# Kernel tuning notes

Measured on AMD Instinct MI355X. Metric: run time of the kernel, lower is better.

The kernel has to match this reference:

```python
import jax, jax.numpy as jnp
import numpy as np

EMBED_DIM = 1024
NUM_HEADS = 16
HEAD_SIZE = EMBED_DIM // NUM_HEADS  # 64
MAX_EMBED_DIM = 2048
MAX_HEAD_SIZE = 128
B, T = 4, 2048


def setup_inputs() -> dict:
    key = jax.random.key(0)
    kx, kq, kk, kv = jax.random.split(key, 4)
    x = jax.random.normal(kx, (B, T, MAX_EMBED_DIM), dtype=jnp.float32)
    # base-head weights sized for the max config; slices are taken in reference()
    Wq = jax.random.normal(kq, (NUM_HEADS, MAX_HEAD_SIZE, MAX_EMBED_DIM), dtype=jnp.float32) * 0.02
    Wk = jax.random.normal(kk, (NUM_HEADS, MAX_HEAD_SIZE, MAX_EMBED_DIM), dtype=jnp.float32) * 0.02
    Wv = jax.random.normal(kv, (NUM_HEADS, MAX_HEAD_SIZE, MAX_EMBED_DIM), dtype=jnp.float32) * 0.02
    return {"x": x, "Wq": Wq, "Wk": Wk, "Wv": Wv}


def reference(x, Wq, Wk, Wv):
    Bx, Tx, _ = x.shape
    xs = x[:, :, :EMBED_DIM]                       # [B, T, E]
    # slice sampled sub-weights: [H, d, E]
    wq = Wq[:, :HEAD_SIZE, :EMBED_DIM]
    wk = Wk[:, :HEAD_SIZE, :EMBED_DIM]
    wv = Wv[:, :HEAD_SIZE, :EMBED_DIM]
    q = jnp.einsum('bte,hde->bhtd', xs, wq)        # [B, H, T, d]
    k = jnp.einsum('bte,hde->bhtd', xs, wk)
    v = jnp.einsum('bte,hde->bhtd', xs, wv)
    scale = jnp.asarray(HEAD_SIZE, x.dtype) ** -0.5
    wei = jnp.einsum('bhtd,bhsd->bhts', q, k) * scale   # [B, H, T, T]
    causal = jnp.tril(jnp.ones((Tx, Tx), dtype=bool))
    wei = jnp.where(causal, wei, jnp.asarray(-jnp.inf, wei.dtype))
    wei = jax.nn.softmax(wei, axis=-1)
    # dropout is identity in eval mode
    out = jnp.einsum('bhts,bhsd->bhtd', wei, v)    # [B, H, T, d]
    out = out.transpose(0, 2, 1, 3).reshape(Bx, Tx, NUM_HEADS * HEAD_SIZE)
    pad = MAX_EMBED_DIM - NUM_HEADS * HEAD_SIZE
    return jnp.pad(out, ((0, 0), (0, 0), (0, pad)))
```

## Files before the change

### kernel.cpp

```cpp
#include <hip/hip_runtime.h>

typedef __attribute__((ext_vector_type(8))) short bf16x8;
typedef __attribute__((ext_vector_type(4))) float f32x4;
typedef __attribute__((ext_vector_type(16))) float f32x16;
typedef __attribute__((ext_vector_type(8))) unsigned short u16x8;
typedef __attribute__((ext_vector_type(4))) unsigned int u32x4;

#define TT 2048

__device__ __forceinline__ unsigned short f2bf(float f) {
  unsigned int u = __builtin_bit_cast(unsigned int, f);
  u += 0x7FFFu + ((u >> 16) & 1u);
  return (unsigned short)(u >> 16);
}

__device__ __forceinline__ void gld16(const void* g, void* l) {
  __builtin_amdgcn_global_load_lds((const __attribute__((address_space(1))) void*)g,
                                   (__attribute__((address_space(3))) void*)l, 16, 0, 0);
}

__device__ __forceinline__ unsigned int cvtpk(float lo, float hi) {
  unsigned int r;
  asm("v_cvt_pk_bf16_f32 %0, %1, %2" : "=v"(r) : "v"(lo), "v"(hi));
  return r;
}

__device__ __forceinline__ void pl32swap(unsigned int& a, unsigned int& b) {
  asm volatile("v_permlane32_swap_b32 %0, %1" : "+v"(a), "+v"(b));
}

__global__ __launch_bounds__(256) void conv_all(const float* __restrict__ x,
                                                const float* __restrict__ Wq,
                                                const float* __restrict__ Wk,
                                                const float* __restrict__ Wv,
                                                unsigned short* __restrict__ xb,
                                                unsigned short* __restrict__ wb) {
  const int bid = blockIdx.x;
  const float* src;
  unsigned short* dst;
  size_t idx;
  if (bid < 4096) {
    idx = ((size_t)bid * 256 + threadIdx.x) * 8;
    const int m = (int)(idx >> 10);
    const int e = (int)(idx & 1023);
    src = x + (size_t)m * 2048 + e;
    dst = xb + idx;
  } else {
    idx = ((size_t)(bid - 4096) * 256 + threadIdx.x) * 8;
    const int n = (int)(idx >> 10);
    const int e = (int)(idx & 1023);
    const int mat = n >> 10, hh = (n >> 6) & 15, d = n & 63;
    const float* W = (mat == 0) ? Wq : ((mat == 1) ? Wk : Wv);
    src = W + ((size_t)hh * 128 + d) * 2048 + e;
    dst = wb + idx;
  }
  const float4* s = (const float4*)src;
  float4 a = s[0], b = s[1];
  u16x8 v;
  v[0]=f2bf(a.x); v[1]=f2bf(a.y); v[2]=f2bf(a.z); v[3]=f2bf(a.w);
  v[4]=f2bf(b.x); v[5]=f2bf(b.y); v[6]=f2bf(b.z); v[7]=f2bf(b.w);
  *(u16x8*)dst = v;
}

__global__ __launch_bounds__(256, 3) void qkv_gemm5(const unsigned short* __restrict__ xb,
                                                    const unsigned short* __restrict__ wb,
                                                    unsigned short* __restrict__ Q,
                                                    unsigned short* __restrict__ Kt,
                                                    unsigned short* __restrict__ Vt) {
  __shared__ unsigned short As[3][64 * 64];
  __shared__ unsigned short Bs[3][64 * 64];
  const int tid = threadIdx.x;
  const int w = tid >> 6, lane = tid & 63, g = lane >> 4, c = lane & 15;
  const int wm = w >> 1, wn = w & 1;
  const int m0 = blockIdx.x * 128;
  const int n0 = blockIdx.y * 128;

  size_t aoff[2], boff[2];
  int lofs[2];
#pragma unroll
  for (int it = 0; it < 2; ++it) {
    const int o = (it * 256 + tid) * 16;
    const int row = o >> 7, stored = o & 127;
    const int logical = stored ^ ((row & 7) << 4);
    const int seg = logical >> 6, kb = logical & 63;
    const int m = row + (seg << 6);
    aoff[it] = ((size_t)(m0 + m) << 10) + (kb >> 1);
    boff[it] = ((size_t)(n0 + m) << 10) + (kb >> 1);
    lofs[it] = o;
  }
  int ardo[4], brdo[4];
#pragma unroll
  for (int mi = 0; mi < 4; ++mi) {
    const int m = wm * 64 + mi * 16 + c;
    const int row = m & 63, seg = m >> 6;
    ardo[mi] = row * 128 + (((seg << 6) + (g << 4)) ^ ((row & 7) << 4));
    const int n = wn * 64 + mi * 16 + c;
    const int nrow = n & 63, nseg = n >> 6;
    brdo[mi] = nrow * 128 + (((nseg << 6) + (g << 4)) ^ ((nrow & 7) << 4));
  }

  f32x4 acc[4][4];
#pragma unroll
  for (int mi = 0; mi < 4; ++mi)
#pragma unroll
    for (int ni = 0; ni < 4; ++ni) acc[mi][ni] = (f32x4){0.f, 0.f, 0.f, 0.f};

  auto STAGE = [&](int k0, int buf) {
#pragma unroll
    for (int it = 0; it < 2; ++it) {
      gld16(xb + aoff[it] + k0, (char*)&As[buf][0] + lofs[it]);
      gld16(wb + boff[it] + k0, (char*)&Bs[buf][0] + lofs[it]);
    }
  };

  STAGE(0, 0);
  STAGE(32, 1);
  asm volatile("s_waitcnt vmcnt(4)" ::: "memory");
  __builtin_amdgcn_s_barrier();

  int b0 = 0, b1 = 1, b2 = 2;
  for (int t = 0; t < 32; ++t) {
    const bool more = (t + 2 < 32);
    if (more) STAGE((t + 2) * 32, b2);
    bf16x8 af[4], bfv[4];
#pragma unroll
    for (int mi = 0; mi < 4; ++mi) {
      af[mi]  = *(const bf16x8*)((const char*)&As[b0][0] + ardo[mi]);
      bfv[mi] = *(const bf16x8*)((const char*)&Bs[b0][0] + brdo[mi]);
    }
    __builtin_amdgcn_s_setprio(1);
#pragma unroll
    for (int mi = 0; mi < 4; ++mi)
#pragma unroll
      for (int ni = 0; ni < 4; ++ni)
        acc[mi][ni] = __builtin_amdgcn_mfma_f32_16x16x32_bf16(af[mi], bfv[ni], acc[mi][ni], 0, 0, 0);
    __builtin_amdgcn_s_setprio(0);
    if (more) asm volatile("s_waitcnt vmcnt(4)" ::: "memory");
    else      asm volatile("s_waitcnt vmcnt(0)" ::: "memory");
    __builtin_amdgcn_s_barrier();
    const int tmp = b0; b0 = b1; b1 = b2; b2 = tmp;
  }

#pragma unroll
  for (int mi = 0; mi < 4; ++mi) {
    const int row_l = wm * 64 + mi * 16 + g * 4;
#pragma unroll
    for (int i = 0; i < 4; ++i) {
      const int m = m0 + row_l + i;
      const int b = m >> 11, tt = m & 2047;
#pragma unroll
      for (int ni = 0; ni < 4; ++ni) {
        const int n = n0 + wn * 64 + ni * 16 + c;
        const int mat = n >> 10, hh = (n >> 6) & 15, d = n & 63;
        const unsigned short v = f2bf(acc[mi][ni][i]);
        const size_t bh = (size_t)(b * 16 + hh);
        if (mat == 0)      Q [(bh * TT + tt) * 64 + d] = v;
        else if (mat == 1) Kt[(bh * TT + tt) * 64 + d] = v;
        else               Vt[(bh * 64 + d) * TT + tt] = v;
      }
    }
  }
}

__global__ __launch_bounds__(256) void attn4(const unsigned short* __restrict__ Q,
                                             const unsigned short* __restrict__ K,
                                             const unsigned short* __restrict__ Vt,
                                             float* __restrict__ out) {
  __shared__ unsigned short Ks[2][4096];
  __shared__ unsigned short Vs[2][4096];
  const int blk = blockIdx.x;
  const int bh = blk & 63;
  const int qi = 15 - (blk >> 6);
  const int b = bh >> 4, h = bh & 15;
  const int tid = threadIdx.x;
  const int w = tid >> 6, lane = tid & 63;
  const int ql = lane & 31;
  const int hi = lane >> 5, hi8 = hi * 8;
  const int q0 = qi * 128;
  const int qw = q0 + w * 32;
  const int q = qw + ql;
  const unsigned short* Qp = Q  + (size_t)bh * TT * 64;
  const unsigned short* Kp = K  + (size_t)bh * TT * 64;
  const unsigned short* Vp = Vt + (size_t)bh * 64 * TT;

  bf16x8 qf0, qf1, qf2, qf3;
  {
    const unsigned short* qa = Qp + (size_t)q * 64 + hi8;
    qf0 = *(const bf16x8*)(qa);
    qf1 = *(const bf16x8*)(qa + 16);
    qf2 = *(const bf16x8*)(qa + 32);
    qf3 = *(const bf16x8*)(qa + 48);
  }

  f32x16 o0, o1;
#pragma unroll
  for (int r = 0; r < 16; ++r) { o0[r] = 0.f; o1[r] = 0.f; }
  float m = -3.0e38f, l = 0.f;
  const float c2 = 0.125f * 1.44269504f;

  const int nt = qi * 2 + 2;

  auto STAGE = [&](int t, int buf) {
#pragma unroll
    for (int it = 0; it < 2; ++it) {
      const int o = (it * 256 + tid) * 16;
      const int r = o >> 7, c = o & 127;
      const int cs = c ^ ((r & 7) << 4);
      gld16(Kp + (size_t)t * 4096 + r * 64 + (cs >> 1), (char*)&Ks[buf][0] + o);
      gld16(Vp + (size_t)r * 2048 + t * 64 + (cs >> 1), (char*)&Vs[buf][0] + o);
    }
  };

  STAGE(0, 0);
  asm volatile("s_waitcnt vmcnt(0)" ::: "memory");
  __syncthreads();

  int cur = 0;
  for (int t = 0; t < nt; ++t) {
    if (t + 1 < nt) STAGE(t + 1, cur ^ 1);

#pragma unroll
    for (int s = 0; s < 2; ++s) {
      const int ks32 = t * 64 + s * 32;
      if (ks32 <= qw) {
        const int krow = s * 32 + ql;
        const char* kb = (const char*)&Ks[cur][krow * 64];
        const int ksz = (krow & 7) << 4;
        bf16x8 kf0 = *(const bf16x8*)(kb + ((0  + hi * 16) ^ ksz));
        bf16x8 kf1 = *(const bf16x8*)(kb + ((32 + hi * 16) ^ ksz));
        bf16x8 kf2 = *(const bf16x8*)(kb + ((64 + hi * 16) ^ ksz));
        bf16x8 kf3 = *(const bf16x8*)(kb + ((96 + hi * 16) ^ ksz));
        const int vsz = (ql & 7) << 4;
        const char* vb0 = (const char*)&Vs[cur][ql * 64];
        const char* vb1 = (const char*)&Vs[cur][(ql + 32) * 64];
        bf16x8 vf0 = *(const bf16x8*)(vb0 + ((s * 64 + 0  + hi * 16) ^ vsz));
        bf16x8 vf1 = *(const bf16x8*)(vb0 + ((s * 64 + 32 + hi * 16) ^ vsz));
        bf16x8 vf2 = *(const bf16x8*)(vb1 + ((s * 64 + 0  + hi * 16) ^ vsz));
        bf16x8 vf3 = *(const bf16x8*)(vb1 + ((s * 64 + 32 + hi * 16) ^ vsz));

        f32x16 st;
#pragma unroll
        for (int r = 0; r < 16; ++r) st[r] = 0.f;
        __builtin_amdgcn_s_setprio(1);
        st = __builtin_amdgcn_mfma_f32_32x32x16_bf16(kf0, qf0, st, 0, 0, 0);
        st = __builtin_amdgcn_mfma_f32_32x32x16_bf16(kf1, qf1, st, 0, 0, 0);
        st = __builtin_amdgcn_mfma_f32_32x32x16_bf16(kf2, qf2, st, 0, 0, 0);
        st = __builtin_amdgcn_mfma_f32_32x32x16_bf16(kf3, qf3, st, 0, 0, 0);
        __builtin_amdgcn_s_setprio(0);

        if (ks32 == qw) {
#pragma unroll
          for (int r = 0; r < 16; ++r) {
            const int krw = (r & 3) + 8 * (r >> 2) + 4 * hi;
            if (krw > ql) st[r] = -3.0e38f;
          }
        }

        float t0 = fmaxf(st[0], st[1]),  t1 = fmaxf(st[2], st[3]);
        float t2 = fmaxf(st[4], st[5]),  t3 = fmaxf(st[6], st[7]);
        float t4 = fmaxf(st[8], st[9]),  t5 = fmaxf(st[10], st[11]);
        float t6 = fmaxf(st[12], st[13]), t7 = fmaxf(st[14], st[15]);
        t0 = fmaxf(t0, t1); t2 = fmaxf(t2, t3); t4 = fmaxf(t4, t5); t6 = fmaxf(t6, t7);
        float pm = fmaxf(fmaxf(t0, t2), fmaxf(t4, t6));
        pm = fmaxf(pm, __shfl_xor(pm, 32));
        if (!__all(pm - m <= 44.36f)) {
          const float mnew = fmaxf(m, pm);
          const float alpha = __builtin_amdgcn_exp2f((m - mnew) * c2);
          m = mnew;
          l *= alpha;
#pragma unroll
          for (int r = 0; r < 16; ++r) { o0[r] *= alpha; o1[r] *= alpha; }
        }
        float p[16];
        float rs = 0.f;
#pragma unroll
        for (int r = 0; r < 16; ++r) {
          p[r] = __builtin_amdgcn_exp2f((st[r] - m) * c2);
          rs += p[r];
        }
        rs += __shfl_xor(rs, 32);
        l += rs;

        unsigned int a0 = cvtpk(p[0], p[1]),  a1 = cvtpk(p[2], p[3]);
        unsigned int b0 = cvtpk(p[4], p[5]),  b1 = cvtpk(p[6], p[7]);
        pl32swap(a0, b0); pl32swap(a1, b1);
        unsigned int cc0 = cvtpk(p[8], p[9]),  cc1 = cvtpk(p[10], p[11]);
        unsigned int dd0 = cvtpk(p[12], p[13]), dd1 = cvtpk(p[14], p[15]);
        pl32swap(cc0, dd0); pl32swap(cc1, dd1);
        u32x4 pw0 = {a0, a1, b0, b1};
        u32x4 pw1 = {cc0, cc1, dd0, dd1};
        bf16x8 pf0 = __builtin_bit_cast(bf16x8, pw0);
        bf16x8 pf1 = __builtin_bit_cast(bf16x8, pw1);

        __builtin_amdgcn_s_setprio(1);
        o0 = __builtin_amdgcn_mfma_f32_32x32x16_bf16(vf0, pf0, o0, 0, 0, 0);
        o0 = __builtin_amdgcn_mfma_f32_32x32x16_bf16(vf1, pf1, o0, 0, 0, 0);
        o1 = __builtin_amdgcn_mfma_f32_32x32x16_bf16(vf2, pf0, o1, 0, 0, 0);
        o1 = __builtin_amdgcn_mfma_f32_32x32x16_bf16(vf3, pf1, o1, 0, 0, 0);
        __builtin_amdgcn_s_setprio(0);
      }
    }

    asm volatile("s_waitcnt vmcnt(0)" ::: "memory");
    __syncthreads();
    cur ^= 1;
  }

  const float inv = 1.f / l;
  float* ob = out + ((size_t)b * TT + q) * 2048 + h * 64;
#pragma unroll
  for (int r = 0; r < 16; ++r) {
    const int row = (r & 3) + 8 * (r >> 2) + 4 * hi;
    ob[row]      = o0[r] * inv;
    ob[32 + row] = o1[r] * inv;
  }

  const float4 z = make_float4(0.f, 0.f, 0.f, 0.f);
#pragma unroll
  for (int it = 0; it < 8; ++it) {
    const int idx = it * 256 + tid;
    const int r = idx >> 4, c4 = idx & 15;
    *((float4*)(out + ((size_t)b * TT + q0 + r) * 2048 + 1024 + h * 64) + c4) = z;
  }
}

extern "C" void kernel_launch(void* const* d_in, const int* in_sizes, int n_in,
                              void* d_out, int out_size, void* d_ws, size_t ws_size,
                              hipStream_t stream) {
  const float* x  = (const float*)d_in[0];
  const float* Wq = (const float*)d_in[1];
  const float* Wk = (const float*)d_in[2];
  const float* Wv = (const float*)d_in[3];

  unsigned short* wsp = (unsigned short*)d_ws;
  unsigned short* Q   = wsp;
  unsigned short* Kt  = wsp + (size_t)8388608;
  unsigned short* Vt  = wsp + (size_t)16777216;

  unsigned short* xb = (unsigned short*)d_out;
  unsigned short* wb = (unsigned short*)((char*)d_out + 33554432);
  float* out = (float*)d_out;

  conv_all<<<5632, 256, 0, stream>>>(x, Wq, Wk, Wv, xb, wb);
  qkv_gemm5<<<dim3(64, 24), 256, 0, stream>>>(xb, wb, Q, Kt, Vt);
  attn4<<<1024, 256, 0, stream>>>(Q, Kt, Vt, out);
}
```

Before: 168.0 us.

## Rewrite QKV GEMM with 256x256 tiles, 8 waves, and interleaved load/MFMA phases

Replaces the 128x128 triple-buffered QKV projection GEMM with a 256x256 tile kernel using 512 threads (8 waves, each computing 128x64) and double-buffered K=64 stages split into four interleaved load/compute phases. A block-index swizzle groups tiles for better L2 reuse of the A and B panels. The larger tile raises arithmetic intensity and cuts redundant global reads. In exchange it uses more registers and LDS per block, adds more barriers per iteration, and launches only 384 blocks, so there is less occupancy to hide latency.

Measured after the change: 175.3 us. 1.04x slower.

```diff
diff --git a/kernel.cpp b/kernel.cpp
--- a/kernel.cpp
+++ b/kernel.cpp
@@ -62,88 +62,135 @@
   *(u16x8*)dst = v;
 }
 
-__global__ __launch_bounds__(256, 3) void qkv_gemm5(const unsigned short* __restrict__ xb,
-                                                    const unsigned short* __restrict__ wb,
-                                                    unsigned short* __restrict__ Q,
-                                                    unsigned short* __restrict__ Kt,
-                                                    unsigned short* __restrict__ Vt) {
-  __shared__ unsigned short As[3][64 * 64];
-  __shared__ unsigned short Bs[3][64 * 64];
+__global__ __launch_bounds__(512) void qkv_gemm8(const unsigned short* __restrict__ xb,
+                                                 const unsigned short* __restrict__ wb,
+                                                 unsigned short* __restrict__ Q,
+                                                 unsigned short* __restrict__ Kt,
+                                                 unsigned short* __restrict__ Vt) {
+  __shared__ unsigned short As[2][2][8192];
+  __shared__ unsigned short Bs[2][2][8192];
   const int tid = threadIdx.x;
   const int w = tid >> 6, lane = tid & 63, g = lane >> 4, c = lane & 15;
-  const int wm = w >> 1, wn = w & 1;
-  const int m0 = blockIdx.x * 128;
-  const int n0 = blockIdx.y * 128;
+  const int wm = w >> 2, wn = w & 3;
+  const int bid = blockIdx.x;
+  const int swz = (bid & 7) * 48 + (bid >> 3);
+  const int m0 = (swz / 12) * 256;
+  const int n0 = (swz % 12) * 256;
 
   size_t aoff[2], boff[2];
   int lofs[2];
 #pragma unroll
   for (int it = 0; it < 2; ++it) {
-    const int o = (it * 256 + tid) * 16;
-    const int row = o >> 7, stored = o & 127;
-    const int logical = stored ^ ((row & 7) << 4);
+    const int o = (it * 512 + tid) * 16;
+    const int lr = o >> 7;
+    const int logical = (o & 127) ^ ((lr & 7) << 4);
     const int seg = logical >> 6, kb = logical & 63;
-    const int m = row + (seg << 6);
-    aoff[it] = ((size_t)(m0 + m) << 10) + (kb >> 1);
-    boff[it] = ((size_t)(n0 + m) << 10) + (kb >> 1);
+    const int r = lr + (seg << 7);
+    aoff[it] = (size_t)(m0 + r) * 1024 + (kb >> 1);
+    boff[it] = (size_t)(n0 + r) * 1024 + (kb >> 1);
     lofs[it] = o;
   }
-  int ardo[4], brdo[4];
-#pragma unroll
-  for (int mi = 0; mi < 4; ++mi) {
-    const int m = wm * 64 + mi * 16 + c;
-    const int row = m & 63, seg = m >> 6;
-    ardo[mi] = row * 128 + (((seg << 6) + (g << 4)) ^ ((row & 7) << 4));
-    const int n = wn * 64 + mi * 16 + c;
-    const int nrow = n & 63, nseg = n >> 6;
-    brdo[mi] = nrow * 128 + (((nseg << 6) + (g << 4)) ^ ((nrow & 7) << 4));
-  }
-
-  f32x4 acc[4][4];
-#pragma unroll
-  for (int mi = 0; mi < 4; ++mi)
+  int abyte[8], bbyte[4];
+#pragma unroll
+  for (int mi = 0; mi < 8; ++mi) {
+    const int r = wm * 128 + mi * 16 + c;
+    abyte[mi] = ((r & 127) << 7) + ((((r >> 7) << 6) + (g << 4)) ^ ((r & 7) << 4));
+  }
+#pragma unroll
+  for (int ni = 0; ni < 4; ++ni) {
+    const int n = wn * 64 + ni * 16 + c;
+    bbyte[ni] = ((n & 127) << 7) + ((((n >> 7) << 6) + (g << 4)) ^ ((n & 7) << 4));
+  }
+
+  f32x4 acc[8][4];
+#pragma unroll
+  for (int mi = 0; mi < 8; ++mi)
 #pragma unroll
     for (int ni = 0; ni < 4; ++ni) acc[mi][ni] = (f32x4){0.f, 0.f, 0.f, 0.f};
 
-  auto STAGE = [&](int k0, int buf) {
-#pragma unroll
-    for (int it = 0; it < 2; ++it) {
-      gld16(xb + aoff[it] + k0, (char*)&As[buf][0] + lofs[it]);
-      gld16(wb + boff[it] + k0, (char*)&Bs[buf][0] + lofs[it]);
-    }
+  auto SA = [&](int t, int kk, int e) {
+#pragma unroll
+    for (int it = 0; it < 2; ++it)
+      gld16(xb + aoff[it] + t * 64 + kk * 32, (char*)&As[e][kk][0] + lofs[it]);
   };
-
-  STAGE(0, 0);
-  STAGE(32, 1);
+  auto SB = [&](int t, int kk, int e) {
+#pragma unroll
+    for (int it = 0; it < 2; ++it)
+      gld16(wb + boff[it] + t * 64 + kk * 32, (char*)&Bs[e][kk][0] + lofs[it]);
+  };
+
+  SA(0, 0, 0); SB(0, 0, 0); SA(0, 1, 0); SB(0, 1, 0);
   asm volatile("s_waitcnt vmcnt(4)" ::: "memory");
   __builtin_amdgcn_s_barrier();
 
-  int b0 = 0, b1 = 1, b2 = 2;
-  for (int t = 0; t < 32; ++t) {
-    const bool more = (t + 2 < 32);
-    if (more) STAGE((t + 2) * 32, b2);
-    bf16x8 af[4], bfv[4];
-#pragma unroll
-    for (int mi = 0; mi < 4; ++mi) {
-      af[mi]  = *(const bf16x8*)((const char*)&As[b0][0] + ardo[mi]);
-      bfv[mi] = *(const bf16x8*)((const char*)&Bs[b0][0] + brdo[mi]);
-    }
+  for (int t = 0; t < 16; ++t) {
+    const int d = t & 1, e = d ^ 1;
+    const bool more = (t + 1 < 16);
+    bf16x8 bf[4], bg[4], a0[4], a1[4], a2[4], a3[4];
+
+    if (more) SA(t + 1, 0, e);
+#pragma unroll
+    for (int ni = 0; ni < 4; ++ni) bf[ni] = *(const bf16x8*)((const char*)&Bs[d][0][0] + bbyte[ni]);
+#pragma unroll
+    for (int mi = 0; mi < 4; ++mi) a0[mi] = *(const bf16x8*)((const char*)&As[d][0][0] + abyte[mi]);
+    __builtin_amdgcn_s_barrier();
     __builtin_amdgcn_s_setprio(1);
 #pragma unroll
     for (int mi = 0; mi < 4; ++mi)
 #pragma unroll
       for (int ni = 0; ni < 4; ++ni)
-        acc[mi][ni] = __builtin_amdgcn_mfma_f32_16x16x32_bf16(af[mi], bfv[ni], acc[mi][ni], 0, 0, 0);
+        acc[mi][ni] = __builtin_amdgcn_mfma_f32_16x16x32_bf16(a0[mi], bf[ni], acc[mi][ni], 0, 0, 0);
     __builtin_amdgcn_s_setprio(0);
+    __builtin_amdgcn_s_barrier();
+
+    if (more) SB(t + 1, 0, e);
+#pragma unroll
+    for (int mi = 0; mi < 4; ++mi) a1[mi] = *(const bf16x8*)((const char*)&As[d][0][0] + abyte[mi + 4]);
     if (more) asm volatile("s_waitcnt vmcnt(4)" ::: "memory");
     else      asm volatile("s_waitcnt vmcnt(0)" ::: "memory");
     __builtin_amdgcn_s_barrier();
-    const int tmp = b0; b0 = b1; b1 = b2; b2 = tmp;
-  }
-
-#pragma unroll
-  for (int mi = 0; mi < 4; ++mi) {
-    const int row_l = wm * 64 + mi * 16 + g * 4;
+    __builtin_amdgcn_s_setprio(1);
+#pragma unroll
+    for (int mi = 0; mi < 4; ++mi)
+#pragma unroll
+      for (int ni = 0; ni < 4; ++ni)
+        acc[mi + 4][ni] = __builtin_amdgcn_mfma_f32_16x16x32_bf16(a1[mi], bf[ni], acc[mi + 4][ni], 0, 0, 0);
+    __builtin_amdgcn_s_setprio(0);
+    __builtin_amdgcn_s_barrier();
+
+    if (more) SA(t + 1, 1, e);
+#pragma unroll
+    for (int ni = 0; ni < 4; ++ni) bg[ni] = *(const bf16x8*)((const char*)&Bs[d][1][0] + bbyte[ni]);
+#pragma unroll
+    for (int mi = 0; mi < 4; ++mi) a2[mi] = *(const bf16x8*)((const char*)&As[d][1][0] + abyte[mi]);
+    __builtin_amdgcn_s_barrier();
+    __builtin_amdgcn_s_setprio(1);
+#pragma unroll
+    for (int mi = 0; mi < 4; ++mi)
+#pragma unroll
+      for (int ni = 0; ni < 4; ++ni)
+        acc[mi][ni] = __builtin_amdgcn_mfma_f32_16x16x32_bf16(a2[mi], bg[ni], acc[mi][ni], 0, 0, 0);
+    __builtin_amdgcn_s_setprio(0);
+    __builtin_amdgcn_s_barrier();
+
+    if (more) SB(t + 1, 1, e);
+#pragma unroll
+    for (int mi = 0; mi < 4; ++mi) a3[mi] = *(const bf16x8*)((const char*)&As[d][1][0] + abyte[mi + 4]);
+    if (more) asm volatile("s_waitcnt vmcnt(4)" ::: "memory");
+    __builtin_amdgcn_s_barrier();
+    __builtin_amdgcn_s_setprio(1);
+#pragma unroll
+    for (int mi = 0; mi < 4; ++mi)
+#pragma unroll
+      for (int ni = 0; ni < 4; ++ni)
+        acc[mi + 4][ni] = __builtin_amdgcn_mfma_f32_16x16x32_bf16(a3[mi], bg[ni], acc[mi + 4][ni], 0, 0, 0);
+    __builtin_amdgcn_s_setprio(0);
+    __builtin_amdgcn_s_barrier();
+  }
+
+#pragma unroll
+  for (int mi = 0; mi < 8; ++mi) {
+    const int row_l = wm * 128 + mi * 16 + g * 4;
 #pragma unroll
     for (int i = 0; i < 4; ++i) {
       const int m = m0 + row_l + i;
@@ -151,12 +198,12 @@
 #pragma unroll
       for (int ni = 0; ni < 4; ++ni) {
         const int n = n0 + wn * 64 + ni * 16 + c;
-        const int mat = n >> 10, hh = (n >> 6) & 15, d = n & 63;
+        const int mat = n >> 10, hh = (n >> 6) & 15, d2 = n & 63;
         const unsigned short v = f2bf(acc[mi][ni][i]);
         const size_t bh = (size_t)(b * 16 + hh);
-        if (mat == 0)      Q [(bh * TT + tt) * 64 + d] = v;
-        else if (mat == 1) Kt[(bh * TT + tt) * 64 + d] = v;
-        else               Vt[(bh * 64 + d) * TT + tt] = v;
+        if (mat == 0)      Q [(bh * TT + tt) * 64 + d2] = v;
+        else if (mat == 1) Kt[(bh * TT + tt) * 64 + d2] = v;
+        else               Vt[(bh * 64 + d2) * TT + tt] = v;
       }
     }
   }
@@ -342,6 +389,6 @@
   float* out = (float*)d_out;
 
   conv_all<<<5632, 256, 0, stream>>>(x, Wq, Wk, Wv, xb, wb);
-  qkv_gemm5<<<dim3(64, 24), 256, 0, stream>>>(xb, wb, Q, Kt, Vt);
+  qkv_gemm8<<<384, 512, 0, stream>>>(xb, wb, Q, Kt, Vt);
   attn4<<<1024, 256, 0, stream>>>(Q, Kt, Vt, out);
 }
```

## Deepen GEMM prefetch pipeline and enlarge attention blocks with triple-buffered K/V

Applied to the files above, without the earlier changes.

The QKV GEMM moves from a 3-stage to a 5-buffer LDS ring with three tiles in flight, and occupancy hint 2, to hide more global-load latency. The attention kernel now uses 512-thread blocks covering 256 query rows, so each K/V tile staged in LDS is shared by twice as many waves. It also triple-buffers K/V with counted vmcnt waits, replacing a full drain every iteration. The cost is more LDS per block and lower occupancy. Causal load balance also gets coarser with half as many attention blocks.

Result: no change. 165.1 us (-1.8%).

```diff
diff --git a/kernel.cpp b/kernel.cpp
--- a/kernel.cpp
+++ b/kernel.cpp
@@ -62,13 +62,13 @@
   *(u16x8*)dst = v;
 }
 
-__global__ __launch_bounds__(256, 3) void qkv_gemm5(const unsigned short* __restrict__ xb,
+__global__ __launch_bounds__(256, 2) void qkv_gemm9(const unsigned short* __restrict__ xb,
                                                     const unsigned short* __restrict__ wb,
                                                     unsigned short* __restrict__ Q,
                                                     unsigned short* __restrict__ Kt,
                                                     unsigned short* __restrict__ Vt) {
-  __shared__ unsigned short As[3][64 * 64];
-  __shared__ unsigned short Bs[3][64 * 64];
+  __shared__ unsigned short As[5][64 * 64];
+  __shared__ unsigned short Bs[5][64 * 64];
   const int tid = threadIdx.x;
   const int w = tid >> 6, lane = tid & 63, g = lane >> 4, c = lane & 15;
   const int wm = w >> 1, wn = w & 1;
@@ -115,13 +115,13 @@
 
   STAGE(0, 0);
   STAGE(32, 1);
-  asm volatile("s_waitcnt vmcnt(4)" ::: "memory");
+  STAGE(64, 2);
+  asm volatile("s_waitcnt vmcnt(8)" ::: "memory");
   __builtin_amdgcn_s_barrier();
 
-  int b0 = 0, b1 = 1, b2 = 2;
+  int b0 = 0, b1 = 1, b2 = 2, b3 = 3, b4 = 4;
   for (int t = 0; t < 32; ++t) {
-    const bool more = (t + 2 < 32);
-    if (more) STAGE((t + 2) * 32, b2);
+    if (t + 3 < 32) STAGE((t + 3) * 32, b3);
     bf16x8 af[4], bfv[4];
 #pragma unroll
     for (int mi = 0; mi < 4; ++mi) {
@@ -135,10 +135,11 @@
       for (int ni = 0; ni < 4; ++ni)
         acc[mi][ni] = __builtin_amdgcn_mfma_f32_16x16x32_bf16(af[mi], bfv[ni], acc[mi][ni], 0, 0, 0);
     __builtin_amdgcn_s_setprio(0);
-    if (more) asm volatile("s_waitcnt vmcnt(4)" ::: "memory");
-    else      asm volatile("s_waitcnt vmcnt(0)" ::: "memory");
+    if (t + 3 < 32)      asm volatile("s_waitcnt vmcnt(8)" ::: "memory");
+    else if (t + 2 < 32) asm volatile("s_waitcnt vmcnt(4)" ::: "memory");
+    else if (t + 1 < 32) asm volatile("s_waitcnt vmcnt(0)" ::: "memory");
     __builtin_amdgcn_s_barrier();
-    const int tmp = b0; b0 = b1; b1 = b2; b2 = tmp;
+    const int tmp = b0; b0 = b1; b1 = b2; b2 = b3; b3 = b4; b4 = tmp;
   }
 
 #pragma unroll
@@ -162,21 +163,21 @@
   }
 }
 
-__global__ __launch_bounds__(256) void attn4(const unsigned short* __restrict__ Q,
-                                             const unsigned short* __restrict__ K,
-                                             const unsigned short* __restrict__ Vt,
-                                             float* __restrict__ out) {
-  __shared__ unsigned short Ks[2][4096];
-  __shared__ unsigned short Vs[2][4096];
+__global__ __launch_bounds__(512, 2) void attn5(const unsigned short* __restrict__ Q,
+                                                const unsigned short* __restrict__ K,
+                                                const unsigned short* __restrict__ Vt,
+                                                float* __restrict__ out) {
+  __shared__ unsigned short Ks[3][4096];
+  __shared__ unsigned short Vs[3][4096];
   const int blk = blockIdx.x;
   const int bh = blk & 63;
-  const int qi = 15 - (blk >> 6);
+  const int qi = 7 - (blk >> 6);
   const int b = bh >> 4, h = bh & 15;
   const int tid = threadIdx.x;
   const int w = tid >> 6, lane = tid & 63;
   const int ql = lane & 31;
   const int hi = lane >> 5, hi8 = hi * 8;
-  const int q0 = qi * 128;
+  const int q0 = qi * 256;
   const int qw = q0 + w * 32;
   const int q = qw + ql;
   const unsigned short* Qp = Q  + (size_t)bh * TT * 64;
@@ -198,41 +199,39 @@
   float m = -3.0e38f, l = 0.f;
   const float c2 = 0.125f * 1.44269504f;
 
-  const int nt = qi * 2 + 2;
+  const int nt = qi * 4 + 4;
 
   auto STAGE = [&](int t, int buf) {
-#pragma unroll
-    for (int it = 0; it < 2; ++it) {
-      const int o = (it * 256 + tid) * 16;
-      const int r = o >> 7, c = o & 127;
-      const int cs = c ^ ((r & 7) << 4);
-      gld16(Kp + (size_t)t * 4096 + r * 64 + (cs >> 1), (char*)&Ks[buf][0] + o);
-      gld16(Vp + (size_t)r * 2048 + t * 64 + (cs >> 1), (char*)&Vs[buf][0] + o);
-    }
+    const int o = tid * 16;
+    const int r = o >> 7, c = o & 127;
+    const int cs = c ^ ((r & 7) << 4);
+    gld16(Kp + (size_t)t * 4096 + r * 64 + (cs >> 1), (char*)&Ks[buf][0] + o);
+    gld16(Vp + (size_t)r * 2048 + t * 64 + (cs >> 1), (char*)&Vs[buf][0] + o);
   };
 
   STAGE(0, 0);
-  asm volatile("s_waitcnt vmcnt(0)" ::: "memory");
-  __syncthreads();
-
-  int cur = 0;
+  STAGE(1, 1);
+  asm volatile("s_waitcnt vmcnt(2)" ::: "memory");
+  __builtin_amdgcn_s_barrier();
+
+  int c0 = 0, c1 = 1, c2x = 2;
   for (int t = 0; t < nt; ++t) {
-    if (t + 1 < nt) STAGE(t + 1, cur ^ 1);
+    if (t + 2 < nt) STAGE(t + 2, c2x);
 
 #pragma unroll
     for (int s = 0; s < 2; ++s) {
       const int ks32 = t * 64 + s * 32;
       if (ks32 <= qw) {
         const int krow = s * 32 + ql;
-        const char* kb = (const char*)&Ks[cur][krow * 64];
+        const char* kb = (const char*)&Ks[c0][krow * 64];
         const int ksz = (krow & 7) << 4;
         bf16x8 kf0 = *(const bf16x8*)(kb + ((0  + hi * 16) ^ ksz));
         bf16x8 kf1 = *(const bf16x8*)(kb + ((32 + hi * 16) ^ ksz));
         bf16x8 kf2 = *(const bf16x8*)(kb + ((64 + hi * 16) ^ ksz));
         bf16x8 kf3 = *(const bf16x8*)(kb + ((96 + hi * 16) ^ ksz));
         const int vsz = (ql & 7) << 4;
-        const char* vb0 = (const char*)&Vs[cur][ql * 64];
-        const char* vb1 = (const char*)&Vs[cur][(ql + 32) * 64];
+        const char* vb0 = (const char*)&Vs[c0][ql * 64];
+        const char* vb1 = (const char*)&Vs[c0][(ql + 32) * 64];
         bf16x8 vf0 = *(const bf16x8*)(vb0 + ((s * 64 + 0  + hi * 16) ^ vsz));
         bf16x8 vf1 = *(const bf16x8*)(vb0 + ((s * 64 + 32 + hi * 16) ^ vsz));
         bf16x8 vf2 = *(const bf16x8*)(vb1 + ((s * 64 + 0  + hi * 16) ^ vsz));
@@ -301,9 +300,10 @@
       }
     }
 
-    asm volatile("s_waitcnt vmcnt(0)" ::: "memory");
-    __syncthreads();
-    cur ^= 1;
+    if (t + 2 < nt)      asm volatile("s_waitcnt vmcnt(2)" ::: "memory");
+    else if (t + 1 < nt) asm volatile("s_waitcnt vmcnt(0)" ::: "memory");
+    __builtin_amdgcn_s_barrier();
+    const int tmp = c0; c0 = c1; c1 = c2x; c2x = tmp;
   }
 
   const float inv = 1.f / l;
@@ -318,7 +318,7 @@
   const float4 z = make_float4(0.f, 0.f, 0.f, 0.f);
 #pragma unroll
   for (int it = 0; it < 8; ++it) {
-    const int idx = it * 256 + tid;
+    const int idx = it * 512 + tid;
     const int r = idx >> 4, c4 = idx & 15;
     *((float4*)(out + ((size_t)b * TT + q0 + r) * 2048 + 1024 + h * 64) + c4) = z;
   }
@@ -342,6 +342,6 @@
   float* out = (float*)d_out;
 
   conv_all<<<5632, 256, 0, stream>>>(x, Wq, Wk, Wv, xb, wb);
-  qkv_gemm5<<<dim3(64, 24), 256, 0, stream>>>(xb, wb, Q, Kt, Vt);
-  attn4<<<1024, 256, 0, stream>>>(Q, Kt, Vt, out);
-}
+  qkv_gemm9<<<dim3(64, 24), 256, 0, stream>>>(xb, wb, Q, Kt, Vt);
+  attn5<<<512, 512, 0, stream>>>(Q, Kt, Vt, out);
+}
```
